# Performance work log

Measured on AMD Instinct MI355X. Metric: run time of the kernel, lower is better.

The kernel has to match this reference:

```python
import jax, jax.numpy as jnp
import numpy as np

B, T, ENC, DEC, OUT = 512, 128, 256, 256, 1
Tm1 = T - 1


def setup_inputs() -> dict:
    key = jax.random.key(0)
    ks = jax.random.split(key, 14)
    s = lambda k, shape, scale=0.05: (jax.random.normal(k, shape, dtype=jnp.float32) * scale)
    return {
        "input_encoded": jax.random.normal(ks[0], (B, Tm1, ENC), dtype=jnp.float32),
        "y_history": jax.random.normal(ks[1], (B, Tm1, OUT), dtype=jnp.float32),
        # attn_layer: Linear(2*DEC+ENC -> ENC), Tanh, Linear(ENC -> 1)
        "W_attn1": s(ks[2], (ENC, 2 * DEC + ENC)),
        "b_attn1": s(ks[3], (ENC,)),
        "W_attn2": s(ks[4], (1, ENC)),
        "b_attn2": s(ks[5], (1,)),
        # single-layer LSTM cell (input_size=OUT, hidden=DEC); gate order i,f,g,o
        "W_ih": s(ks[6], (4 * DEC, OUT)),
        "W_hh": s(ks[7], (4 * DEC, DEC)),
        "b_ih": s(ks[8], (4 * DEC,)),
        "b_hh": s(ks[9], (4 * DEC,)),
        # fc: Linear(ENC+OUT -> OUT); torch code re-inits weight ~ N(0,1)
        "W_fc": jax.random.normal(ks[10], (OUT, ENC + OUT), dtype=jnp.float32),
        "b_fc": s(ks[11], (OUT,)),
        # fc_final: Linear(DEC+ENC -> OUT)
        "W_fcf": s(ks[12], (OUT, DEC + ENC)),
        "b_fcf": s(ks[13], (OUT,)),
    }


def reference(input_encoded, y_history, W_attn1, b_attn1, W_attn2, b_attn2,
              W_ih, W_hh, b_ih, b_hh, W_fc, b_fc, W_fcf, b_fcf):
    Bsz, tm1, enc = input_encoded.shape
    dec = W_hh.shape[1]
    h0 = jnp.zeros((Bsz, dec), dtype=input_encoded.dtype)
    c0 = jnp.zeros_like(h0)
    ctx0 = jnp.zeros((Bsz, enc), dtype=input_encoded.dtype)

    def step(carry, y_t):
        h, c, _ = carry  # h, c: [B, DEC]; y_t: [B, OUT]
        hs = jnp.broadcast_to(h[:, None, :], (Bsz, tm1, dec))
        cs = jnp.broadcast_to(c[:, None, :], (Bsz, tm1, dec))
        x = jnp.concatenate([hs, cs, input_encoded], axis=-1)  # [B, Tm1, 2*DEC+ENC]
        score = jnp.tanh(x @ W_attn1.T + b_attn1) @ W_attn2.T + b_attn2  # [B, Tm1, 1]
        attn = jax.nn.softmax(score[..., 0], axis=1)  # [B, Tm1]
        context = jnp.einsum('bt,bte->be', attn, input_encoded)  # [B, ENC]
        y_tilde = jnp.concatenate([context, y_t], axis=1) @ W_fc.T + b_fc  # [B, OUT]
        gates = y_tilde @ W_ih.T + b_ih + h @ W_hh.T + b_hh  # [B, 4*DEC]
        i, f, g, o = jnp.split(gates, 4, axis=1)
        c_new = jax.nn.sigmoid(f) * c + jax.nn.sigmoid(i) * jnp.tanh(g)
        h_new = jax.nn.sigmoid(o) * jnp.tanh(c_new)
        return (h_new, c_new, context), attn

    (h, c, context), attn_rows = jax.lax.scan(
        step, (h0, c0, ctx0), jnp.swapaxes(y_history, 0, 1))
    weight = jnp.swapaxes(attn_rows, 0, 1)  # [B, Tm1, Tm1]
    out = jnp.concatenate([h, context], axis=1) @ W_fcf.T + b_fcf  # [B, OUT]
    return out, weight
```

## Files before the change

kernel.cpp:

```cpp
#include <hip/hip_runtime.h>

typedef _Float16 f16;
typedef _Float16 h2 __attribute__((ext_vector_type(2)));
typedef _Float16 h4 __attribute__((ext_vector_type(4)));
typedef _Float16 h8 __attribute__((ext_vector_type(8)));

#define T127 127

__device__ __forceinline__ float rcp_f(float x) { return __builtin_amdgcn_rcpf(x); }

__device__ __forceinline__ float fdot2(h2 a, h2 b, float c) {
  return __builtin_amdgcn_fdot2(a, b, c, false);
}
__device__ __forceinline__ h2 mk2(f16 a, f16 b) { h2 v; v[0] = a; v[1] = b; return v; }

__device__ __forceinline__ float fast_tanh(float x) {
  x = fminf(fmaxf(x, -12.f), 12.f);
  float e = __expf(2.f * x);
  return (e - 1.f) * rcp_f(e + 1.f);
}
__device__ __forceinline__ float fast_sig(float x) {
  x = fminf(fmaxf(x, -30.f), 30.f);
  return rcp_f(1.f + __expf(-x));
}

__global__ void pack_wa1c(const float* __restrict__ Wa1, f16* __restrict__ wsA) {
  int tid = blockIdx.x * 256 + threadIdx.x;
  int it = tid >> 9, L = tid & 511;
  int k = L >> 1, g2 = L & 1;
  const float* src = Wa1 + (size_t)k * 768 + 256 + g2 * 128 + it * 8;
  f16* dst = wsA + (size_t)tid * 8;
#pragma unroll
  for (int j = 0; j < 8; ++j) dst[j] = (f16)src[j];
}

__global__ void pack_whh2(const float* __restrict__ Whh, f16* __restrict__ wsH) {
  int tid = blockIdx.x * 256 + threadIdx.x;
  int m = tid >> 9, L = tid & 511;
  int row = L + (m & 1) * 512;
  int it = m >> 1;
  const float* src = Whh + (size_t)row * 256 + it * 8;
  f16* dst = wsH + (size_t)tid * 8;
#pragma unroll
  for (int j = 0; j < 8; ++j) dst[j] = (f16)src[j];
}

__global__ __attribute__((amdgpu_flat_work_group_size(512, 512)))
void decoder_kernel(
    const float* __restrict__ enc,
    const float* __restrict__ yhist,
    const float* __restrict__ Wa1,
    const float* __restrict__ ba1,
    const float* __restrict__ Wa2,
    const float* __restrict__ ba2,
    const float* __restrict__ Wih,
    const float* __restrict__ bih,
    const float* __restrict__ bhh,
    const float* __restrict__ Wfc,
    const float* __restrict__ bfc,
    const float* __restrict__ Wfcf,
    const float* __restrict__ bfcf,
    const f16* __restrict__ wsA,
    const f16* __restrict__ wsH,
    float* __restrict__ outp)
{
  __shared__ __align__(16) f16 tE1[2][T127][280];
  __shared__ __align__(16) f16 hch[2][4][136];
  __shared__ __align__(16) float s_arr[2][4][68];
  __shared__ __align__(16) float score_s[2][128];
  __shared__ __align__(16) float p_s[2][128];
  __shared__ __align__(16) float q_s[2][128];
  __shared__ __align__(16) char ovl[8192];
  __shared__ __align__(16) float w2_lds[256];
  __shared__ __align__(16) float yh_s[2][128];
  __shared__ float ctxq_s[2], red[8];

  float* gact = (float*)ovl;
  f16* est = (f16*)ovl;

  const int L = threadIdx.x;
  const int b0 = blockIdx.x * 2;
  const int kL = L >> 1;
  const int g2 = L & 1;

  for (int i = L; i < 1088; i += 512) ((f16*)hch)[i] = (f16)0.f;
  if (L < 256) {
    w2_lds[L] = Wa2[L];
    int bb = L >> 7, tt = L & 127;
    if (tt < T127) yh_s[bb][tt] = yhist[(size_t)(b0 + bb) * T127 + tt];
  }
  float c_reg = 0.f;

  {
    h2 we1[64];
    {
      const float4* wrow = (const float4*)(Wa1 + (size_t)kL * 768 + 512 + g2 * 128);
#pragma unroll
      for (int i = 0; i < 32; ++i) {
        float4 w = wrow[i];
        we1[2 * i]     = mk2((f16)w.x, (f16)w.y);
        we1[2 * i + 1] = mk2((f16)w.z, (f16)w.w);
      }
    }
    const int prow = L >> 6;
    const int lm = L & 63;
    const int sg = lm >> 4;
    const int si = (lm * 4) & 63;

#pragma unroll 1
    for (int tt = 0; tt < 32; ++tt) {
      __syncthreads();
      {
        int bbs = prow >> 2, j4 = prow & 3, j = tt * 4 + j4;
        float4 v = make_float4(0.f, 0.f, 0.f, 0.f);
        if (j < T127)
          v = *(const float4*)(enc + (((size_t)(b0 + bbs)) * T127 + j) * 256 + lm * 4);
        h4 hv; hv[0] = (f16)v.x; hv[1] = (f16)v.y; hv[2] = (f16)v.z; hv[3] = (f16)v.w;
        *(h4*)(est + prow * 288 + sg * 72 + si) = hv;
      }
      __syncthreads();
#pragma unroll 1
      for (int P = 0; P < 8; ++P) {
        int bbs = P >> 2, j4 = P & 3, j = tt * 4 + j4;
        const h8* ep = (const h8*)(est + P * 288 + (2 * g2) * 72);
        const h8* ep2 = (const h8*)(est + P * 288 + (2 * g2 + 1) * 72);
        float a0 = 0.f, a1 = 0.f;
#pragma unroll
        for (int r = 0; r < 8; ++r) {
          h8 e8 = ep[r];
          a0 = fdot2(we1[4 * r + 0], mk2(e8[0], e8[1]), a0);
          a1 = fdot2(we1[4 * r + 1], mk2(e8[2], e8[3]), a1);
          a0 = fdot2(we1[4 * r + 2], mk2(e8[4], e8[5]), a0);
          a1 = fdot2(we1[4 * r + 3], mk2(e8[6], e8[7]), a1);
        }
#pragma unroll
        for (int r = 0; r < 8; ++r) {
          h8 e8 = ep2[r];
          a0 = fdot2(we1[32 + 4 * r + 0], mk2(e8[0], e8[1]), a0);
          a1 = fdot2(we1[32 + 4 * r + 1], mk2(e8[2], e8[3]), a1);
          a0 = fdot2(we1[32 + 4 * r + 2], mk2(e8[4], e8[5]), a0);
          a1 = fdot2(we1[32 + 4 * r + 3], mk2(e8[6], e8[7]), a1);
        }
        float acc = a0 + a1;
        acc += __shfl_xor(acc, 1, 64);
        if (g2 == 0 && j < T127)
          tE1[bbs][j][(kL >> 6) * 68 + (kL & 63)] = (f16)fast_tanh(acc);
      }
      {
        int bbs = prow >> 2, j4 = prow & 3, j = tt * 4 + j4;
        float4 wp4 = *(const float4*)(Wfc + lm * 4);
        float4 wq4 = *(const float4*)(Wfcf + 256 + lm * 4);
        h4 ev = *(const h4*)(est + prow * 288 + sg * 72 + si);
        float pacc = (float)ev[0] * wp4.x + (float)ev[1] * wp4.y + (float)ev[2] * wp4.z + (float)ev[3] * wp4.w;
        float qacc = (float)ev[0] * wq4.x + (float)ev[1] * wq4.y + (float)ev[2] * wq4.z + (float)ev[3] * wq4.w;
#pragma unroll
        for (int s = 32; s; s >>= 1) {
          pacc += __shfl_xor(pacc, s, 64);
          qacc += __shfl_xor(qacc, s, 64);
        }
        if (lm == 0 && j < T127) { p_s[bbs][j] = pacc; q_s[bbs][j] = qacc; }
      }
    }
  }
  __syncthreads();

  h2 w1h[64];
  {
    const float4* wrow = (const float4*)(Wa1 + (size_t)kL * 768 + g2 * 128);
#pragma unroll
    for (int i = 0; i < 32; ++i) {
      float4 w = wrow[i];
      w1h[2 * i]     = mk2((f16)w.x, (f16)w.y);
      w1h[2 * i + 1] = mk2((f16)w.z, (f16)w.w);
    }
  }
  const float b1k = ba1[kL];
  const float wihA = Wih[L];
  const float wihB = Wih[512 + L];
  const float biasA = bih[L] + bhh[L];
  const float biasB = bih[512 + L] + bhh[512 + L];
  const float ba2v = ba2[0];
  const float wfcy = Wfc[256];
  const float bfc0 = bfc[0];
  const int g_u = L & 3;
  __syncthreads();

#pragma unroll 1
  for (int t = 0; t < T127; ++t) {
    const h8* wA = (const h8*)wsA + L;
    const h8* wH = (const h8*)wsH + L;
    h8 a0 = wA[0], a1 = wA[512];
    h8 p0 = wH[0], p1 = wH[512];

    float u0a = 0.f, u0b = 0.f, u1a = 0.f, u1b = 0.f;
    {
      const h8* hp0 = (const h8*)&hch[0][g2][0];
      const h8* hp1 = (const h8*)&hch[1][g2][0];
#pragma unroll
      for (int r = 0; r < 16; ++r) {
        h8 x = hp0[r];
        u0a = fdot2(w1h[4 * r + 0], mk2(x[0], x[1]), u0a);
        u0b = fdot2(w1h[4 * r + 1], mk2(x[2], x[3]), u0b);
        u0a = fdot2(w1h[4 * r + 2], mk2(x[4], x[5]), u0a);
        u0b = fdot2(w1h[4 * r + 3], mk2(x[6], x[7]), u0b);
        h8 y = hp1[r];
        u1a = fdot2(w1h[4 * r + 0], mk2(y[0], y[1]), u1a);
        u1b = fdot2(w1h[4 * r + 1], mk2(y[2], y[3]), u1b);
        u1a = fdot2(w1h[4 * r + 2], mk2(y[4], y[5]), u1a);
        u1b = fdot2(w1h[4 * r + 3], mk2(y[6], y[7]), u1b);
      }
    }
    {
      const h8* cp0 = (const h8*)&hch[0][2 + g2][0];
      const h8* cp1 = (const h8*)&hch[1][2 + g2][0];
#pragma unroll 1
      for (int it = 0; it < 16; ++it) {
        h8 nxt = wA[((it + 2) & 15) * 512];
        h8 c0 = cp0[it], c1 = cp1[it];
        u0a = fdot2(mk2(a0[0], a0[1]), mk2(c0[0], c0[1]), u0a);
        u0b = fdot2(mk2(a0[2], a0[3]), mk2(c0[2], c0[3]), u0b);
        u0a = fdot2(mk2(a0[4], a0[5]), mk2(c0[4], c0[5]), u0a);
        u0b = fdot2(mk2(a0[6], a0[7]), mk2(c0[6], c0[7]), u0b);
        u1a = fdot2(mk2(a0[0], a0[1]), mk2(c1[0], c1[1]), u1a);
        u1b = fdot2(mk2(a0[2], a0[3]), mk2(c1[2], c1[3]), u1b);
        u1a = fdot2(mk2(a0[4], a0[5]), mk2(c1[4], c1[5]), u1a);
        u1b = fdot2(mk2(a0[6], a0[7]), mk2(c1[6], c1[7]), u1b);
        a0 = a1; a1 = nxt;
      }
    }
    {
      float u0 = u0a + u0b, u1 = u1a + u1b;
      u0 += __shfl_xor(u0, 1, 64);
      u1 += __shfl_xor(u1, 1, 64);
      if (g2 == 0) s_arr[0][kL >> 6][kL & 63] = fast_tanh(u0 + b1k);
      else         s_arr[1][kL >> 6][kL & 63] = fast_tanh(u1 + b1k);
    }
    __syncthreads();

    float ghA0 = 0.f, ghA1 = 0.f, ghB0 = 0.f, ghB1 = 0.f;
    float acc0 = 0.f, acc1 = 0.f;
    int pr = L >> 2;
    int bbB = pr & 1, jB = pr >> 1;
    const h4* tp = (const h4*)&tE1[bbB][jB][g_u * 68];
    const float4* sp = (const float4*)&s_arr[bbB][g_u][0];
    const float4* w2p = (const float4*)&w2_lds[g_u * 64];
#pragma unroll 1
    for (int i = 0; i < 32; ++i) {
      int m = 2 * i;
      h8 n0 = wH[((m + 2) & 63) * 512];
      h8 n1 = wH[((m + 3) & 63) * 512];
      int ch = i >> 4, off = (i & 15) * 8;
      h8 x = *(const h8*)&hch[0][ch][off];
      h8 y = *(const h8*)&hch[1][ch][off];
      ghA0 = fdot2(mk2(p0[0], p0[1]), mk2(x[0], x[1]), ghA0);
      ghA0 = fdot2(mk2(p0[2], p0[3]), mk2(x[2], x[3]), ghA0);
      ghA0 = fdot2(mk2(p0[4], p0[5]), mk2(x[4], x[5]), ghA0);
      ghA0 = fdot2(mk2(p0[6], p0[7]), mk2(x[6], x[7]), ghA0);
      ghA1 = fdot2(mk2(p0[0], p0[1]), mk2(y[0], y[1]), ghA1);
      ghA1 = fdot2(mk2(p0[2], p0[3]), mk2(y[2], y[3]), ghA1);
      ghA1 = fdot2(mk2(p0[4], p0[5]), mk2(y[4], y[5]), ghA1);
      ghA1 = fdot2(mk2(p0[6], p0[7]), mk2(y[6], y[7]), ghA1);
      ghB0 = fdot2(mk2(p1[0], p1[1]), mk2(x[0], x[1]), ghB0);
      ghB0 = fdot2(mk2(p1[2], p1[3]), mk2(x[2], x[3]), ghB0);
      ghB0 = fdot2(mk2(p1[4], p1[5]), mk2(x[4], x[5]), ghB0);
      ghB0 = fdot2(mk2(p1[6], p1[7]), mk2(x[6], x[7]), ghB0);
      ghB1 = fdot2(mk2(p1[0], p1[1]), mk2(y[0], y[1]), ghB1);
      ghB1 = fdot2(mk2(p1[2], p1[3]), mk2(y[2], y[3]), ghB1);
      ghB1 = fdot2(mk2(p1[4], p1[5]), mk2(y[4], y[5]), ghB1);
      ghB1 = fdot2(mk2(p1[6], p1[7]), mk2(y[6], y[7]), ghB1);
      {
        int ii = i & 15;
        h4 tv = tp[ii];
        float4 sv = sp[ii];
        float4 wv = w2p[ii];
        float t0 = (float)tv[0], t1 = (float)tv[1], t2 = (float)tv[2], t3 = (float)tv[3];
        acc0 = fmaf(wv.x * (sv.x + t0), rcp_f(fmaf(sv.x, t0, 1.f)), acc0);
        acc1 = fmaf(wv.y * (sv.y + t1), rcp_f(fmaf(sv.y, t1, 1.f)), acc1);
        acc0 = fmaf(wv.z * (sv.z + t2), rcp_f(fmaf(sv.z, t2, 1.f)), acc0);
        acc1 = fmaf(wv.w * (sv.w + t3), rcp_f(fmaf(sv.w, t3, 1.f)), acc1);
        if (ii == 15) {
          float acc = acc0 + acc1;
          acc += __shfl_xor(acc, 1, 64);
          acc += __shfl_xor(acc, 2, 64);
          if (g_u == 0 && pr < 254) score_s[bbB][jB] = acc + ba2v;
          acc0 = 0.f; acc1 = 0.f;
          pr = (L >> 2) + 128;
          int prc = (pr < 254) ? pr : 253;
          bbB = prc & 1; jB = prc >> 1;
          tp = (const h4*)&tE1[bbB][jB][g_u * 68];
          sp = (const float4*)&s_arr[bbB][g_u][0];
        }
      }
      p0 = n0; p1 = n1;
    }
    __syncthreads();

    float ytil0, ytil1;
    {
      const int ln = L & 63;
      const int wv = L >> 6;
#pragma unroll
      for (int bb = 0; bb < 2; ++bb) {
        float x0 = score_s[bb][ln];
        float e0 = __expf(x0);
        float e1 = (ln < 63) ? __expf(score_s[bb][64 + ln]) : 0.f;
        float ssum = e0 + e1;
#pragma unroll
        for (int s = 32; s; s >>= 1) ssum += __shfl_xor(ssum, s, 64);
        float rs = rcp_f(ssum);
        float aa0 = e0 * rs, aa1 = e1 * rs;
        if (wv == bb) {
          float* wout = outp + 512 + ((size_t)(b0 + bb) * T127 + t) * T127;
          wout[ln] = aa0;
          if (ln < 63) wout[64 + ln] = aa1;
        }
        float cw = aa0 * p_s[bb][ln] + ((ln < 63) ? aa1 * p_s[bb][64 + ln] : 0.f);
#pragma unroll
        for (int s = 32; s; s >>= 1) cw += __shfl_xor(cw, s, 64);
        float yt = cw + wfcy * yh_s[bb][t] + bfc0;
        if (bb == 0) ytil0 = yt; else ytil1 = yt;
        if (t == T127 - 1) {
          float cq = aa0 * q_s[bb][ln] + ((ln < 63) ? aa1 * q_s[bb][64 + ln] : 0.f);
#pragma unroll
          for (int s = 32; s; s >>= 1) cq += __shfl_xor(cq, s, 64);
          if (L == 0) ctxq_s[bb] = cq;
        }
      }
    }

    {
      float gA0 = ghA0 + wihA * ytil0 + biasA;
      float gA1 = ghA1 + wihA * ytil1 + biasA;
      float gB0 = ghB0 + wihB * ytil0 + biasB;
      float gB1 = ghB1 + wihB * ytil1 + biasB;
      float aA0 = fast_sig(gA0), aA1 = fast_sig(gA1);
      bool isg = (L < 256);
      float aB0 = isg ? fast_tanh(gB0) : fast_sig(gB0);
      float aB1 = isg ? fast_tanh(gB1) : fast_sig(gB1);
      gact[0 * 1024 + L] = aA0;
      gact[1 * 1024 + L] = aA1;
      gact[0 * 1024 + 512 + L] = aB0;
      gact[1 * 1024 + 512 + L] = aB1;
    }
    __syncthreads();

    {
      const int bb = L >> 8, kk = L & 255;
      float gi = gact[bb * 1024 + kk];
      float gf = gact[bb * 1024 + 256 + kk];
      float gg = gact[bb * 1024 + 512 + kk];
      float go = gact[bb * 1024 + 768 + kk];
      float cn = gf * c_reg + gi * gg;
      float hn = go * fast_tanh(cn);
      c_reg = cn;
      hch[bb][kk >> 7][kk & 127] = (f16)hn;
      hch[bb][2 + (kk >> 7)][kk & 127] = (f16)cn;
      if (t == T127 - 1) {
        float po = Wfcf[kk] * hn;
#pragma unroll
        for (int s = 32; s; s >>= 1) po += __shfl_xor(po, s, 64);
        if ((L & 63) == 0) red[L >> 6] = po;
      }
    }
    __syncthreads();
  }

  if (L < 2) {
    float o = red[L * 4] + red[L * 4 + 1] + red[L * 4 + 2] + red[L * 4 + 3] + ctxq_s[L] + bfcf[0];
    outp[b0 + L] = o;
  }
}

extern "C" void kernel_launch(void* const* d_in, const int* in_sizes, int n_in,
                              void* d_out, int out_size, void* d_ws, size_t ws_size,
                              hipStream_t stream) {
  (void)in_sizes; (void)n_in; (void)out_size; (void)ws_size;
  f16* wsA = (f16*)d_ws;
  f16* wsH = wsA + 65536;
  pack_wa1c<<<32, 256, 0, stream>>>((const float*)d_in[2], wsA);
  pack_whh2<<<128, 256, 0, stream>>>((const float*)d_in[7], wsH);
  decoder_kernel<<<256, 512, 0, stream>>>(
      (const float*)d_in[0], (const float*)d_in[1], (const float*)d_in[2],
      (const float*)d_in[3], (const float*)d_in[4], (const float*)d_in[5],
      (const float*)d_in[6], (const float*)d_in[8], (const float*)d_in[9],
      (const float*)d_in[10], (const float*)d_in[11], (const float*)d_in[12],
      (const float*)d_in[13], wsA, wsH, (float*)d_out);
}
```

Measured before the change: 1.825 ms.

## Remap LSTM gate work per thread and stream attention h-weights from workspace

```diff
diff --git a/kernel.cpp b/kernel.cpp
--- a/kernel.cpp
+++ b/kernel.cpp
@@ -24,22 +24,22 @@
   return rcp_f(1.f + __expf(-x));
 }
 
-__global__ void pack_wa1c(const float* __restrict__ Wa1, f16* __restrict__ wsA) {
+__global__ void pack_wsU(const float* __restrict__ Wa1, f16* __restrict__ wsU) {
   int tid = blockIdx.x * 256 + threadIdx.x;
   int it = tid >> 9, L = tid & 511;
-  int k = L >> 1, g2 = L & 1;
-  const float* src = Wa1 + (size_t)k * 768 + 256 + g2 * 128 + it * 8;
-  f16* dst = wsA + (size_t)tid * 8;
+  int kL = L >> 1, g2 = L & 1;
+  const float* src = Wa1 + (size_t)kL * 768 + (it >> 4) * 256 + g2 * 128 + (it & 15) * 8;
+  f16* dst = wsU + (size_t)tid * 8;
 #pragma unroll
   for (int j = 0; j < 8; ++j) dst[j] = (f16)src[j];
 }
 
-__global__ void pack_whh2(const float* __restrict__ Whh, f16* __restrict__ wsH) {
+__global__ void pack_wsH(const float* __restrict__ Whh, f16* __restrict__ wsH) {
   int tid = blockIdx.x * 256 + threadIdx.x;
-  int m = tid >> 9, L = tid & 511;
-  int row = L + (m & 1) * 512;
-  int it = m >> 1;
-  const float* src = Whh + (size_t)row * 256 + it * 8;
+  int m = tid >> 8;
+  int kk = tid & 255;
+  int i = m >> 2, g = m & 3;
+  const float* src = Whh + (size_t)(g * 256 + kk) * 256 + i * 8;
   f16* dst = wsH + (size_t)tid * 8;
 #pragma unroll
   for (int j = 0; j < 8; ++j) dst[j] = (f16)src[j];
@@ -60,7 +60,7 @@
     const float* __restrict__ bfc,
     const float* __restrict__ Wfcf,
     const float* __restrict__ bfcf,
-    const f16* __restrict__ wsA,
+    const f16* __restrict__ wsU,
     const f16* __restrict__ wsH,
     float* __restrict__ outp)
 {
@@ -70,18 +70,18 @@
   __shared__ __align__(16) float score_s[2][128];
   __shared__ __align__(16) float p_s[2][128];
   __shared__ __align__(16) float q_s[2][128];
-  __shared__ __align__(16) char ovl[8192];
+  __shared__ __align__(16) f16 est[8][288];
   __shared__ __align__(16) float w2_lds[256];
   __shared__ __align__(16) float yh_s[2][128];
-  __shared__ float ctxq_s[2], red[8];
-
-  float* gact = (float*)ovl;
-  f16* est = (f16*)ovl;
+  __shared__ float ctxq_s[2], red2[16];
 
   const int L = threadIdx.x;
   const int b0 = blockIdx.x * 2;
   const int kL = L >> 1;
   const int g2 = L & 1;
+  const int kk2 = L >> 1;
+  const int bbE = L & 1;
+  const int g_u = L & 3;
 
   for (int i = L; i < 1088; i += 512) ((f16*)hch)[i] = (f16)0.f;
   if (L < 256) {
@@ -116,14 +116,14 @@
         if (j < T127)
           v = *(const float4*)(enc + (((size_t)(b0 + bbs)) * T127 + j) * 256 + lm * 4);
         h4 hv; hv[0] = (f16)v.x; hv[1] = (f16)v.y; hv[2] = (f16)v.z; hv[3] = (f16)v.w;
-        *(h4*)(est + prow * 288 + sg * 72 + si) = hv;
+        *(h4*)(&est[prow][0] + sg * 72 + si) = hv;
       }
       __syncthreads();
 #pragma unroll 1
       for (int P = 0; P < 8; ++P) {
         int bbs = P >> 2, j4 = P & 3, j = tt * 4 + j4;
-        const h8* ep = (const h8*)(est + P * 288 + (2 * g2) * 72);
-        const h8* ep2 = (const h8*)(est + P * 288 + (2 * g2 + 1) * 72);
+        const h8* ep = (const h8*)(&est[P][0] + (2 * g2) * 72);
+        const h8* ep2 = (const h8*)(&est[P][0] + (2 * g2 + 1) * 72);
         float a0 = 0.f, a1 = 0.f;
 #pragma unroll
         for (int r = 0; r < 8; ++r) {
@@ -150,7 +150,7 @@
         int bbs = prow >> 2, j4 = prow & 3, j = tt * 4 + j4;
         float4 wp4 = *(const float4*)(Wfc + lm * 4);
         float4 wq4 = *(const float4*)(Wfcf + 256 + lm * 4);
-        h4 ev = *(const h4*)(est + prow * 288 + sg * 72 + si);
+        h4 ev = *(const h4*)(&est[prow][0] + sg * 72 + si);
         float pacc = (float)ev[0] * wp4.x + (float)ev[1] * wp4.y + (float)ev[2] * wp4.z + (float)ev[3] * wp4.w;
         float qacc = (float)ev[0] * wq4.x + (float)ev[1] * wq4.y + (float)ev[2] * wq4.z + (float)ev[3] * wq4.w;
 #pragma unroll
@@ -164,68 +164,45 @@
   }
   __syncthreads();
 
-  h2 w1h[64];
-  {
-    const float4* wrow = (const float4*)(Wa1 + (size_t)kL * 768 + g2 * 128);
-#pragma unroll
-    for (int i = 0; i < 32; ++i) {
-      float4 w = wrow[i];
-      w1h[2 * i]     = mk2((f16)w.x, (f16)w.y);
-      w1h[2 * i + 1] = mk2((f16)w.z, (f16)w.w);
-    }
-  }
   const float b1k = ba1[kL];
-  const float wihA = Wih[L];
-  const float wihB = Wih[512 + L];
-  const float biasA = bih[L] + bhh[L];
-  const float biasB = bih[512 + L] + bhh[512 + L];
+  const float wih0 = Wih[kk2];
+  const float wih1 = Wih[256 + kk2];
+  const float wih2 = Wih[512 + kk2];
+  const float wih3 = Wih[768 + kk2];
+  const float bia0 = bih[kk2] + bhh[kk2];
+  const float bia1 = bih[256 + kk2] + bhh[256 + kk2];
+  const float bia2 = bih[512 + kk2] + bhh[512 + kk2];
+  const float bia3 = bih[768 + kk2] + bhh[768 + kk2];
   const float ba2v = ba2[0];
   const float wfcy = Wfc[256];
   const float bfc0 = bfc[0];
-  const int g_u = L & 3;
-  __syncthreads();
+  const float wfcf_k = Wfcf[kk2];
+  const f16* hbase = (const f16*)hch + bbE * 544;
 
 #pragma unroll 1
   for (int t = 0; t < T127; ++t) {
-    const h8* wA = (const h8*)wsA + L;
-    const h8* wH = (const h8*)wsH + L;
-    h8 a0 = wA[0], a1 = wA[512];
-    h8 p0 = wH[0], p1 = wH[512];
+    const h8* wU = (const h8*)wsU + L;
+    const h8* wHp = (const h8*)wsH + kk2;
 
     float u0a = 0.f, u0b = 0.f, u1a = 0.f, u1b = 0.f;
     {
-      const h8* hp0 = (const h8*)&hch[0][g2][0];
-      const h8* hp1 = (const h8*)&hch[1][g2][0];
-#pragma unroll
-      for (int r = 0; r < 16; ++r) {
-        h8 x = hp0[r];
-        u0a = fdot2(w1h[4 * r + 0], mk2(x[0], x[1]), u0a);
-        u0b = fdot2(w1h[4 * r + 1], mk2(x[2], x[3]), u0b);
-        u0a = fdot2(w1h[4 * r + 2], mk2(x[4], x[5]), u0a);
-        u0b = fdot2(w1h[4 * r + 3], mk2(x[6], x[7]), u0b);
-        h8 y = hp1[r];
-        u1a = fdot2(w1h[4 * r + 0], mk2(y[0], y[1]), u1a);
-        u1b = fdot2(w1h[4 * r + 1], mk2(y[2], y[3]), u1b);
-        u1a = fdot2(w1h[4 * r + 2], mk2(y[4], y[5]), u1a);
-        u1b = fdot2(w1h[4 * r + 3], mk2(y[6], y[7]), u1b);
-      }
-    }
-    {
-      const h8* cp0 = (const h8*)&hch[0][2 + g2][0];
-      const h8* cp1 = (const h8*)&hch[1][2 + g2][0];
-#pragma unroll 1
-      for (int it = 0; it < 16; ++it) {
-        h8 nxt = wA[((it + 2) & 15) * 512];
-        h8 c0 = cp0[it], c1 = cp1[it];
-        u0a = fdot2(mk2(a0[0], a0[1]), mk2(c0[0], c0[1]), u0a);
-        u0b = fdot2(mk2(a0[2], a0[3]), mk2(c0[2], c0[3]), u0b);
-        u0a = fdot2(mk2(a0[4], a0[5]), mk2(c0[4], c0[5]), u0a);
-        u0b = fdot2(mk2(a0[6], a0[7]), mk2(c0[6], c0[7]), u0b);
-        u1a = fdot2(mk2(a0[0], a0[1]), mk2(c1[0], c1[1]), u1a);
-        u1b = fdot2(mk2(a0[2], a0[3]), mk2(c1[2], c1[3]), u1b);
-        u1a = fdot2(mk2(a0[4], a0[5]), mk2(c1[4], c1[5]), u1a);
-        u1b = fdot2(mk2(a0[6], a0[7]), mk2(c1[6], c1[7]), u1b);
-        a0 = a1; a1 = nxt;
+      h8 a0 = wU[0], a1 = wU[512], a2 = wU[1024], a3 = wU[1536];
+#pragma unroll 4
+      for (int it = 0; it < 32; ++it) {
+        h8 nxt = wU[((it + 4) & 31) * 512];
+        int ch = (it >> 4) * 2 + g2;
+        const f16* hp = (const f16*)hch + ch * 136 + (it & 15) * 8;
+        h8 x = *(const h8*)hp;
+        h8 y = *(const h8*)(hp + 544);
+        u0a = fdot2(mk2(a0[0], a0[1]), mk2(x[0], x[1]), u0a);
+        u0b = fdot2(mk2(a0[2], a0[3]), mk2(x[2], x[3]), u0b);
+        u0a = fdot2(mk2(a0[4], a0[5]), mk2(x[4], x[5]), u0a);
+        u0b = fdot2(mk2(a0[6], a0[7]), mk2(x[6], x[7]), u0b);
+        u1a = fdot2(mk2(a0[0], a0[1]), mk2(y[0], y[1]), u1a);
+        u1b = fdot2(mk2(a0[2], a0[3]), mk2(y[2], y[3]), u1b);
+        u1a = fdot2(mk2(a0[4], a0[5]), mk2(y[4], y[5]), u1a);
+        u1b = fdot2(mk2(a0[6], a0[7]), mk2(y[6], y[7]), u1b);
+        a0 = a1; a1 = a2; a2 = a3; a3 = nxt;
       }
     }
     {
@@ -237,136 +214,149 @@
     }
     __syncthreads();
 
-    float ghA0 = 0.f, ghA1 = 0.f, ghB0 = 0.f, ghB1 = 0.f;
+    float gh0 = 0.f, gh1 = 0.f, gh2 = 0.f, gh3 = 0.f;
     float acc0 = 0.f, acc1 = 0.f;
     int pr = L >> 2;
     int bbB = pr & 1, jB = pr >> 1;
     const h4* tp = (const h4*)&tE1[bbB][jB][g_u * 68];
     const float4* sp = (const float4*)&s_arr[bbB][g_u][0];
     const float4* w2p = (const float4*)&w2_lds[g_u * 64];
+    h8 A0 = wHp[0], A1 = wHp[256], A2 = wHp[512], A3 = wHp[768];
+    h8 B0 = wHp[1024], B1 = wHp[1280], B2 = wHp[1536], B3 = wHp[1792];
+
+#define FUSED_BODY(C0, C1, C2, C3, IDX)                                        \
+    {                                                                          \
+      int ip = ((IDX) + 2) & 31;                                               \
+      h8 T0 = wHp[(ip * 4 + 0) * 256], T1 = wHp[(ip * 4 + 1) * 256];           \
+      h8 T2 = wHp[(ip * 4 + 2) * 256], T3 = wHp[(ip * 4 + 3) * 256];           \
+      h8 x = *(const h8*)(hbase + ((IDX) >> 4) * 136 + ((IDX) & 15) * 8);      \
+      gh0 = fdot2(mk2(C0[0], C0[1]), mk2(x[0], x[1]), gh0);                    \
+      gh0 = fdot2(mk2(C0[2], C0[3]), mk2(x[2], x[3]), gh0);                    \
+      gh0 = fdot2(mk2(C0[4], C0[5]), mk2(x[4], x[5]), gh0);                    \
+      gh0 = fdot2(mk2(C0[6], C0[7]), mk2(x[6], x[7]), gh0);                    \
+      gh1 = fdot2(mk2(C1[0], C1[1]), mk2(x[0], x[1]), gh1);                    \
+      gh1 = fdot2(mk2(C1[2], C1[3]), mk2(x[2], x[3]), gh1);                    \
+      gh1 = fdot2(mk2(C1[4], C1[5]), mk2(x[4], x[5]), gh1);                    \
+      gh1 = fdot2(mk2(C1[6], C1[7]), mk2(x[6], x[7]), gh1);                    \
+      gh2 = fdot2(mk2(C2[0], C2[1]), mk2(x[0], x[1]), gh2);                    \
+      gh2 = fdot2(mk2(C2[2], C2[3]), mk2(x[2], x[3]), gh2);                    \
+      gh2 = fdot2(mk2(C2[4], C2[5]), mk2(x[4], x[5]), gh2);                    \
+      gh2 = fdot2(mk2(C2[6], C2[7]), mk2(x[6], x[7]), gh2);                    \
+      gh3 = fdot2(mk2(C3[0], C3[1]), mk2(x[0], x[1]), gh3);                    \
+      gh3 = fdot2(mk2(C3[2], C3[3]), mk2(x[2], x[3]), gh3);                    \
+      gh3 = fdot2(mk2(C3[4], C3[5]), mk2(x[4], x[5]), gh3);                    \
+      gh3 = fdot2(mk2(C3[6], C3[7]), mk2(x[6], x[7]), gh3);                    \
+      {                                                                        \
+        int ii = (IDX) & 15;                                                   \
+        h4 tv = tp[ii];                                                        \
+        float4 sv = sp[ii];                                                    \
+        float4 wv2 = w2p[ii];                                                  \
+        float t0 = (float)tv[0], t1 = (float)tv[1];                            \
+        float t2 = (float)tv[2], t3 = (float)tv[3];                            \
+        acc0 = fmaf(wv2.x * (sv.x + t0), rcp_f(fmaf(sv.x, t0, 1.f)), acc0);    \
+        acc1 = fmaf(wv2.y * (sv.y + t1), rcp_f(fmaf(sv.y, t1, 1.f)), acc1);    \
+        acc0 = fmaf(wv2.z * (sv.z + t2), rcp_f(fmaf(sv.z, t2, 1.f)), acc0);    \
+        acc1 = fmaf(wv2.w * (sv.w + t3), rcp_f(fmaf(sv.w, t3, 1.f)), acc1);    \
+        if (ii == 15) {                                                        \
+          float acc = acc0 + acc1;                                             \
+          acc += __shfl_xor(acc, 1, 64);                                       \
+          acc += __shfl_xor(acc, 2, 64);                                       \
+          if (g_u == 0 && pr < 254) score_s[bbB][jB] = acc + ba2v;             \
+          acc0 = 0.f; acc1 = 0.f;                                              \
+          pr = (L >> 2) + 128;                                                 \
+          int prc = (pr < 254) ? pr : 253;                                     \
+          bbB = prc & 1; jB = prc >> 1;                                        \
+          tp = (const h4*)&tE1[bbB][jB][g_u * 68];                             \
+          sp = (const float4*)&s_arr[bbB][g_u][0];                             \
+        }                                                                      \
+      }                                                                        \
+      C0 = T0; C1 = T1; C2 = T2; C3 = T3;                                      \
+    }
+
 #pragma unroll 1
-    for (int i = 0; i < 32; ++i) {
-      int m = 2 * i;
-      h8 n0 = wH[((m + 2) & 63) * 512];
-      h8 n1 = wH[((m + 3) & 63) * 512];
-      int ch = i >> 4, off = (i & 15) * 8;
-      h8 x = *(const h8*)&hch[0][ch][off];
-      h8 y = *(const h8*)&hch[1][ch][off];
-      ghA0 = fdot2(mk2(p0[0], p0[1]), mk2(x[0], x[1]), ghA0);
-      ghA0 = fdot2(mk2(p0[2], p0[3]), mk2(x[2], x[3]), ghA0);
-      ghA0 = fdot2(mk2(p0[4], p0[5]), mk2(x[4], x[5]), ghA0);
-      ghA0 = fdot2(mk2(p0[6], p0[7]), mk2(x[6], x[7]), ghA0);
-      ghA1 = fdot2(mk2(p0[0], p0[1]), mk2(y[0], y[1]), ghA1);
-      ghA1 = fdot2(mk2(p0[2], p0[3]), mk2(y[2], y[3]), ghA1);
-      ghA1 = fdot2(mk2(p0[4], p0[5]), mk2(y[4], y[5]), ghA1);
-      ghA1 = fdot2(mk2(p0[6], p0[7]), mk2(y[6], y[7]), ghA1);
-      ghB0 = fdot2(mk2(p1[0], p1[1]), mk2(x[0], x[1]), ghB0);
-      ghB0 = fdot2(mk2(p1[2], p1[3]), mk2(x[2], x[3]), ghB0);
-      ghB0 = fdot2(mk2(p1[4], p1[5]), mk2(x[4], x[5]), ghB0);
-      ghB0 = fdot2(mk2(p1[6], p1[7]), mk2(x[6], x[7]), ghB0);
-      ghB1 = fdot2(mk2(p1[0], p1[1]), mk2(y[0], y[1]), ghB1);
-      ghB1 = fdot2(mk2(p1[2], p1[3]), mk2(y[2], y[3]), ghB1);
-      ghB1 = fdot2(mk2(p1[4], p1[5]), mk2(y[4], y[5]), ghB1);
-      ghB1 = fdot2(mk2(p1[6], p1[7]), mk2(y[6], y[7]), ghB1);
-      {
-        int ii = i & 15;
-        h4 tv = tp[ii];
-        float4 sv = sp[ii];
-        float4 wv = w2p[ii];
-        float t0 = (float)tv[0], t1 = (float)tv[1], t2 = (float)tv[2], t3 = (float)tv[3];
-        acc0 = fmaf(wv.x * (sv.x + t0), rcp_f(fmaf(sv.x, t0, 1.f)), acc0);
-        acc1 = fmaf(wv.y * (sv.y + t1), rcp_f(fmaf(sv.y, t1, 1.f)), acc1);
-        acc0 = fmaf(wv.z * (sv.z + t2), rcp_f(fmaf(sv.z, t2, 1.f)), acc0);
-        acc1 = fmaf(wv.w * (sv.w + t3), rcp_f(fmaf(sv.w, t3, 1.f)), acc1);
-        if (ii == 15) {
-          float acc = acc0 + acc1;
-          acc += __shfl_xor(acc, 1, 64);
-          acc += __shfl_xor(acc, 2, 64);
-          if (g_u == 0 && pr < 254) score_s[bbB][jB] = acc + ba2v;
-          acc0 = 0.f; acc1 = 0.f;
-          pr = (L >> 2) + 128;
-          int prc = (pr < 254) ? pr : 253;
-          bbB = prc & 1; jB = prc >> 1;
-          tp = (const h4*)&tE1[bbB][jB][g_u * 68];
-          sp = (const float4*)&s_arr[bbB][g_u][0];
-        }
-      }
-      p0 = n0; p1 = n1;
-    }
+    for (int ih = 0; ih < 16; ++ih) {
+      int i0 = 2 * ih;
+      FUSED_BODY(A0, A1, A2, A3, i0)
+      int i1 = 2 * ih + 1;
+      FUSED_BODY(B0, B1, B2, B3, i1)
+    }
+#undef FUSED_BODY
     __syncthreads();
 
     float ytil0, ytil1;
     {
       const int ln = L & 63;
       const int wv = L >> 6;
-#pragma unroll
-      for (int bb = 0; bb < 2; ++bb) {
-        float x0 = score_s[bb][ln];
-        float e0 = __expf(x0);
-        float e1 = (ln < 63) ? __expf(score_s[bb][64 + ln]) : 0.f;
-        float ssum = e0 + e1;
-#pragma unroll
-        for (int s = 32; s; s >>= 1) ssum += __shfl_xor(ssum, s, 64);
-        float rs = rcp_f(ssum);
-        float aa0 = e0 * rs, aa1 = e1 * rs;
-        if (wv == bb) {
-          float* wout = outp + 512 + ((size_t)(b0 + bb) * T127 + t) * T127;
-          wout[ln] = aa0;
-          if (ln < 63) wout[64 + ln] = aa1;
+      float e0a = __expf(score_s[0][ln]);
+      float e1a = (ln < 63) ? __expf(score_s[0][64 + ln]) : 0.f;
+      float e0b = __expf(score_s[1][ln]);
+      float e1b = (ln < 63) ? __expf(score_s[1][64 + ln]) : 0.f;
+      float sa = e0a + e1a, sb = e0b + e1b;
+      float cwa = e0a * p_s[0][ln] + ((ln < 63) ? e1a * p_s[0][64 + ln] : 0.f);
+      float cwb = e0b * p_s[1][ln] + ((ln < 63) ? e1b * p_s[1][64 + ln] : 0.f);
+#pragma unroll
+      for (int s = 32; s; s >>= 1) {
+        sa += __shfl_xor(sa, s, 64);
+        sb += __shfl_xor(sb, s, 64);
+        cwa += __shfl_xor(cwa, s, 64);
+        cwb += __shfl_xor(cwb, s, 64);
+      }
+      float ra = rcp_f(sa), rb = rcp_f(sb);
+      if (wv == 0) {
+        float* wout = outp + 512 + ((size_t)b0 * T127 + t) * T127;
+        wout[ln] = e0a * ra;
+        if (ln < 63) wout[64 + ln] = e1a * ra;
+      } else if (wv == 1) {
+        float* wout = outp + 512 + ((size_t)(b0 + 1) * T127 + t) * T127;
+        wout[ln] = e0b * rb;
+        if (ln < 63) wout[64 + ln] = e1b * rb;
+      }
+      ytil0 = cwa * ra + wfcy * yh_s[0][t] + bfc0;
+      ytil1 = cwb * rb + wfcy * yh_s[1][t] + bfc0;
+      if (t == T127 - 1) {
+        float cqa = e0a * q_s[0][ln] + ((ln < 63) ? e1a * q_s[0][64 + ln] : 0.f);
+        float cqb = e0b * q_s[1][ln] + ((ln < 63) ? e1b * q_s[1][64 + ln] : 0.f);
+#pragma unroll
+        for (int s = 32; s; s >>= 1) {
+          cqa += __shfl_xor(cqa, s, 64);
+          cqb += __shfl_xor(cqb, s, 64);
         }
-        float cw = aa0 * p_s[bb][ln] + ((ln < 63) ? aa1 * p_s[bb][64 + ln] : 0.f);
-#pragma unroll
-        for (int s = 32; s; s >>= 1) cw += __shfl_xor(cw, s, 64);
-        float yt = cw + wfcy * yh_s[bb][t] + bfc0;
-        if (bb == 0) ytil0 = yt; else ytil1 = yt;
-        if (t == T127 - 1) {
-          float cq = aa0 * q_s[bb][ln] + ((ln < 63) ? aa1 * q_s[bb][64 + ln] : 0.f);
-#pragma unroll
-          for (int s = 32; s; s >>= 1) cq += __shfl_xor(cq, s, 64);
-          if (L == 0) ctxq_s[bb] = cq;
-        }
-      }
-    }
-
-    {
-      float gA0 = ghA0 + wihA * ytil0 + biasA;
-      float gA1 = ghA1 + wihA * ytil1 + biasA;
-      float gB0 = ghB0 + wihB * ytil0 + biasB;
-      float gB1 = ghB1 + wihB * ytil1 + biasB;
-      float aA0 = fast_sig(gA0), aA1 = fast_sig(gA1);
-      bool isg = (L < 256);
-      float aB0 = isg ? fast_tanh(gB0) : fast_sig(gB0);
-      float aB1 = isg ? fast_tanh(gB1) : fast_sig(gB1);
-      gact[0 * 1024 + L] = aA0;
-      gact[1 * 1024 + L] = aA1;
-      gact[0 * 1024 + 512 + L] = aB0;
-      gact[1 * 1024 + 512 + L] = aB1;
-    }
-    __syncthreads();
-
-    {
-      const int bb = L >> 8, kk = L & 255;
-      float gi = gact[bb * 1024 + kk];
-      float gf = gact[bb * 1024 + 256 + kk];
-      float gg = gact[bb * 1024 + 512 + kk];
-      float go = gact[bb * 1024 + 768 + kk];
-      float cn = gf * c_reg + gi * gg;
-      float hn = go * fast_tanh(cn);
+        if (L == 0) { ctxq_s[0] = cqa * ra; ctxq_s[1] = cqb * rb; }
+      }
+    }
+
+    {
+      float yt = bbE ? ytil1 : ytil0;
+      float g_i = gh0 + wih0 * yt + bia0;
+      float g_f = gh1 + wih1 * yt + bia1;
+      float g_g = gh2 + wih2 * yt + bia2;
+      float g_o = gh3 + wih3 * yt + bia3;
+      float ai = fast_sig(g_i);
+      float af = fast_sig(g_f);
+      float ag = fast_tanh(g_g);
+      float ao = fast_sig(g_o);
+      float cn = af * c_reg + ai * ag;
+      float hn = ao * fast_tanh(cn);
       c_reg = cn;
-      hch[bb][kk >> 7][kk & 127] = (f16)hn;
-      hch[bb][2 + (kk >> 7)][kk & 127] = (f16)cn;
+      hch[bbE][kk2 >> 7][kk2 & 127] = (f16)hn;
+      hch[bbE][2 + (kk2 >> 7)][kk2 & 127] = (f16)cn;
       if (t == T127 - 1) {
-        float po = Wfcf[kk] * hn;
-#pragma unroll
-        for (int s = 32; s; s >>= 1) po += __shfl_xor(po, s, 64);
-        if ((L & 63) == 0) red[L >> 6] = po;
+        float po = wfcf_k * hn;
+        po += __shfl_xor(po, 32, 64);
+        po += __shfl_xor(po, 16, 64);
+        po += __shfl_xor(po, 8, 64);
+        po += __shfl_xor(po, 4, 64);
+        po += __shfl_xor(po, 2, 64);
+        if ((L & 63) < 2) red2[(L >> 6) * 2 + (L & 1)] = po;
       }
     }
     __syncthreads();
   }
 
   if (L < 2) {
-    float o = red[L * 4] + red[L * 4 + 1] + red[L * 4 + 2] + red[L * 4 + 3] + ctxq_s[L] + bfcf[0];
+    float o = ctxq_s[L] + bfcf[0];
+#pragma unroll
+    for (int w = 0; w < 8; ++w) o += red2[w * 2 + L];
     outp[b0 + L] = o;
   }
 }
@@ -375,14 +365,14 @@
                               void* d_out, int out_size, void* d_ws, size_t ws_size,
                               hipStream_t stream) {
   (void)in_sizes; (void)n_in; (void)out_size; (void)ws_size;
-  f16* wsA = (f16*)d_ws;
-  f16* wsH = wsA + 65536;
-  pack_wa1c<<<32, 256, 0, stream>>>((const float*)d_in[2], wsA);
-  pack_whh2<<<128, 256, 0, stream>>>((const float*)d_in[7], wsH);
+  f16* wsU = (f16*)d_ws;
+  f16* wsH = wsU + 131072;
+  pack_wsU<<<64, 256, 0, stream>>>((const float*)d_in[2], wsU);
+  pack_wsH<<<128, 256, 0, stream>>>((const float*)d_in[7], wsH);
   decoder_kernel<<<256, 512, 0, stream>>>(
       (const float*)d_in[0], (const float*)d_in[1], (const float*)d_in[2],
       (const float*)d_in[3], (const float*)d_in[4], (const float*)d_in[5],
       (const float*)d_in[6], (const float*)d_in[8], (const float*)d_in[9],
       (const float*)d_in[10], (const float*)d_in[11], (const float*)d_in[12],
-      (const float*)d_in[13], wsA, wsH, (float*)d_out);
-}
+      (const float*)d_in[13], wsU, wsH, (float*)d_out);
+}
```

Measured after the change: 1.777 ms. -2.6%, faster.
